# Kernel optimization log

Hardware: AMD Instinct MI355X
Metric: run time of the kernel (lower is better)

## Reference

```python
import jax, jax.numpy as jnp
import numpy as np

EPS = 1e-12


def _l2norm(v):
    return v / (jnp.linalg.norm(v) + EPS)


def _sn(W, u):
    """One-step power-iteration spectral normalization (torch spectral_norm, 1x1 conv weight).
    W: (out, in), u: (out,). u/v are treated as buffers (no grad)."""
    Wm = W.reshape(W.shape[0], -1)
    v = _l2norm(Wm.T @ u)
    u2 = _l2norm(Wm @ v)
    u2 = jax.lax.stop_gradient(u2)
    v = jax.lax.stop_gradient(v)
    sigma = u2 @ (Wm @ v)
    return W / sigma


def _maxpool2(x):
    # 2x2 max pool, stride 2, NCHW
    N, C, H, W = x.shape
    return x.reshape(N, C, H // 2, 2, W // 2, 2).max(axis=(3, 5))


def setup_inputs() -> dict:
    key = jax.random.key(0)
    ks = jax.random.split(key, 10)
    N, C, H, W = 16, 256, 64, 64
    s = 0.05  # keep logits moderate
    return {
        "x": jax.random.normal(ks[0], (N, C, H, W), dtype=jnp.float32),
        "Wt": jax.random.normal(ks[1], (C >> 3, C), dtype=jnp.float32) * s,
        "Wp": jax.random.normal(ks[2], (C >> 3, C), dtype=jnp.float32) * s,
        "Wg": jax.random.normal(ks[3], (C >> 1, C), dtype=jnp.float32) * s,
        "Wo": jax.random.normal(ks[4], (C, C >> 1), dtype=jnp.float32) * s,
        "ut": jax.random.normal(ks[5], (C >> 3,), dtype=jnp.float32),
        "up": jax.random.normal(ks[6], (C >> 3,), dtype=jnp.float32),
        "ug": jax.random.normal(ks[7], (C >> 1,), dtype=jnp.float32),
        "uo": jax.random.normal(ks[8], (C,), dtype=jnp.float32),
        "gamma": jnp.float32(0.1),  # nonzero so attention branch is exercised
    }


def reference(x, Wt, Wp, Wg, Wo, ut, up, ug, uo, gamma):
    N, C, H, W = x.shape
    L = H * W          # location_num
    Ld = L // 4        # downsampled_num
    # 1x1 convs as channel einsums with spectrally-normalized weights
    theta = jnp.einsum('oc,nchw->nohw', _sn(Wt, ut), x).reshape(N, C >> 3, L)
    phi = _maxpool2(jnp.einsum('oc,nchw->nohw', _sn(Wp, up), x)).reshape(N, C >> 3, Ld)
    attn = jax.nn.softmax(jnp.einsum('ncl,ncm->nlm', theta, phi), axis=-1)  # (N, L, Ld)
    g = _maxpool2(jnp.einsum('oc,nchw->nohw', _sn(Wg, ug), x)).reshape(N, C >> 1, Ld)
    attn_g = jnp.einsum('ncm,nlm->ncl', g, attn).reshape(N, C >> 1, H, W)
    attn_g = jnp.einsum('oc,nchw->nohw', _sn(Wo, uo), attn_g)
    return x + gamma * attn_g
```

## Files before the change

kernel.cpp:

```cpp
#include <hip/hip_runtime.h>
#include <math.h>

#define EPS 1e-12f

typedef unsigned short ushort_t;
typedef __attribute__((ext_vector_type(8))) short short8;
typedef __attribute__((ext_vector_type(4))) float f32x4;
typedef __attribute__((ext_vector_type(4))) unsigned short ushort4v;
typedef __attribute__((ext_vector_type(2))) unsigned int uint2v;

#define WS_WB_F 0
#define WS_WO_F 24576
#define WS_TH_F 40960
#define WS_PH_F 1089536
#define WS_G_F  1351680

__device__ __forceinline__ ushort_t f2bf(float f) {
  unsigned int u = __float_as_uint(f);
  u += 0x7fffu + ((u >> 16) & 1u);
  return (ushort_t)(u >> 16);
}
__device__ __forceinline__ float bf2f(ushort_t u) {
  return __uint_as_float(((unsigned int)u) << 16);
}
__device__ __forceinline__ unsigned int pack_bf2(float lo, float hi) {
  return (unsigned int)f2bf(lo) | ((unsigned int)f2bf(hi) << 16);
}

__device__ __forceinline__ void gload_lds16(const ushort_t* g, ushort_t* l) {
  __builtin_amdgcn_global_load_lds(
      (const __attribute__((address_space(1))) unsigned int*)g,
      (__attribute__((address_space(3))) unsigned int*)l, 16, 0, 0);
}

__device__ __forceinline__ float block_reduce_sum(float v, float* red) {
  int t = threadIdx.x;
  red[t] = v;
  __syncthreads();
  #pragma unroll
  for (int s = 128; s > 0; s >>= 1) {
    if (t < s) red[t] += red[t + s];
    __syncthreads();
  }
  float r = red[0];
  __syncthreads();
  return r;
}

__global__ __launch_bounds__(256) void sn_kernel(
    const float* __restrict__ Wt, const float* __restrict__ Wp,
    const float* __restrict__ Wg, const float* __restrict__ Wo,
    const float* __restrict__ ut, const float* __restrict__ up,
    const float* __restrict__ ug, const float* __restrict__ uo,
    float* __restrict__ ws) {
  __shared__ float red[256];
  __shared__ float ub[256];
  __shared__ float vb[256];
  const float* W; const float* u; int O, Ci;
  switch (blockIdx.x) {
    case 0:  W = Wt; u = ut; O = 32;  Ci = 256; break;
    case 1:  W = Wp; u = up; O = 32;  Ci = 256; break;
    case 2:  W = Wg; u = ug; O = 128; Ci = 256; break;
    default: W = Wo; u = uo; O = 256; Ci = 128; break;
  }
  int t = threadIdx.x;
  if (t < O) ub[t] = u[t];
  __syncthreads();
  float tv = 0.f;
  if (t < Ci) {
    for (int o = 0; o < O; o++) tv += W[o * Ci + t] * ub[o];
  }
  float nt2 = block_reduce_sum((t < Ci) ? tv * tv : 0.f, red);
  float ntn = sqrtf(nt2);
  if (t < Ci) vb[t] = tv / (ntn + EPS);
  __syncthreads();
  float sv = 0.f;
  if (t < O) {
    const float* Wr = W + (size_t)t * Ci;
    for (int c = 0; c < Ci; c += 4) {
      float4 wv = *(const float4*)(Wr + c);
      sv += wv.x * vb[c] + wv.y * vb[c + 1] + wv.z * vb[c + 2] + wv.w * vb[c + 3];
    }
  }
  float ss = block_reduce_sum((t < O) ? sv * sv : 0.f, red);
  float ns = sqrtf(ss);
  float sigma = ss / (ns + EPS);
  float inv = 1.f / sigma;
  int total = O * Ci;
  if (blockIdx.x == 3) {
    ushort_t* dst = (ushort_t*)(ws + WS_WO_F);
    for (int i = t; i < total; i += 256) {
      int o = i >> 7, c = i & 127;
      int oct = o >> 4, l16o = o & 15, kc = c >> 5, qd = (c >> 3) & 3, j = c & 7;
      dst[(((kc * 16 + oct) * 64 + qd * 16 + l16o) << 3) + j] = f2bf(W[i] * inv);
    }
  } else {
    int base_row = (blockIdx.x == 0) ? 0 : (blockIdx.x == 1 ? 32 : 64);
    ushort_t* dst = (ushort_t*)(ws + WS_WB_F);
    for (int i = t; i < total; i += 256) {
      int o = i >> 8, c = i & 255;
      int og = base_row + o;
      int mtg = og >> 4, l16o = og & 15, kc = c >> 5, qd = (c >> 3) & 3, j = c & 7;
      dst[(((mtg * 8 + kc) * 64 + qd * 16 + l16o) << 3) + j] = f2bf(W[i] * inv);
    }
  }
}

__global__ __launch_bounds__(256, 2) void proj_mfma(
    const float* __restrict__ x, const ushort_t* __restrict__ wb,
    ushort_t* __restrict__ theta_b, ushort_t* __restrict__ phi_b,
    ushort_t* __restrict__ g_b) {
  __shared__ ushort_t xb[128 * 264];
  const int t = threadIdx.x;
  const int n = blockIdx.y;
  const int l0 = blockIdx.x * 128;
  const float* xn = x + ((size_t)n * 256) * 4096 + l0;
  {
    const int lrel = t & 127;
    const int half = t >> 7;
    #pragma unroll 4
    for (int ch = 0; ch < 16; ++ch) {
      int chunk = half * 16 + ch;
      short8 v;
      #pragma unroll
      for (int j = 0; j < 8; ++j) {
        float f = xn[(size_t)(chunk * 8 + j) * 4096 + lrel];
        v[j] = (short)f2bf(f);
      }
      *(short8*)(&xb[lrel * 264 + chunk * 8]) = v;
    }
  }
  __syncthreads();
  const int w = t >> 6;
  const int lane = t & 63;
  const int quad = lane >> 4;
  const int l16 = lane & 15;
  const int rowA = (w * 16 + l16) * 264;
  const int rowB = (64 + w * 16 + l16) * 264;
  const int hd = blockIdx.x;
  #pragma unroll 1
  for (int pass = 0; pass < 2; ++pass) {
    f32x4 accA[6], accB[6];
    #pragma unroll
    for (int i = 0; i < 6; ++i) {
      accA[i] = (f32x4){0.f, 0.f, 0.f, 0.f};
      accB[i] = (f32x4){0.f, 0.f, 0.f, 0.f};
    }
    #pragma unroll
    for (int kc = 0; kc < 8; ++kc) {
      short8 bA = *(const short8*)(&xb[rowA + kc * 32 + quad * 8]);
      short8 bB = *(const short8*)(&xb[rowB + kc * 32 + quad * 8]);
      #pragma unroll
      for (int mt = 0; mt < 6; ++mt) {
        int mtg = pass * 6 + mt;
        short8 aW = *(const short8*)(wb + (((size_t)(mtg * 8 + kc) * 64 + lane) << 3));
        accA[mt] = __builtin_amdgcn_mfma_f32_16x16x32_bf16(aW, bA, accA[mt], 0, 0, 0);
        accB[mt] = __builtin_amdgcn_mfma_f32_16x16x32_bf16(aW, bB, accB[mt], 0, 0, 0);
      }
    }
    #pragma unroll
    for (int mt = 0; mt < 6; ++mt) {
      int mtg = pass * 6 + mt;
      if (mtg < 2) {
        int lA = l0 + w * 16 + l16;
        ushort4v vA, vB;
        #pragma unroll
        for (int r = 0; r < 4; ++r) { vA[r] = f2bf(accA[mt][r]); vB[r] = f2bf(accB[mt][r]); }
        *(ushort4v*)(theta_b + ((size_t)n * 4096 + lA) * 32 + mtg * 16 + quad * 4) = vA;
        *(ushort4v*)(theta_b + ((size_t)n * 4096 + lA + 64) * 32 + mtg * 16 + quad * 4) = vB;
      } else {
        float pm[4];
        #pragma unroll
        for (int r = 0; r < 4; ++r) {
          float v = fmaxf(accA[mt][r], accB[mt][r]);
          v = fmaxf(v, __shfl_xor(v, 1));
          pm[r] = v;
        }
        if ((l16 & 1) == 0) {
          int m = hd * 32 + w * 8 + (l16 >> 1);
          if (mtg < 4) {
            ushort4v vv;
            #pragma unroll
            for (int r = 0; r < 4; ++r) vv[r] = f2bf(pm[r]);
            *(ushort4v*)(phi_b + ((size_t)n * 1024 + m) * 32 + (mtg - 2) * 16 + quad * 4) = vv;
          } else {
            int cg0 = (mtg - 4) * 16 + quad * 4;
            #pragma unroll
            for (int r = 0; r < 4; ++r)
              g_b[((size_t)n * 128 + cg0 + r) * 1024 + m] = f2bf(pm[r]);
          }
        }
      }
    }
  }
}

__device__ __forceinline__ void stage_g(const ushort_t* gN, ushort_t* buf,
                                        int m0, int w, int l16, int quad) {
  #pragma unroll
  for (int b = 0; b < 8; ++b) {
    int idx = w * 8 + b;
    int j = idx >> 2, s = idx & 3;
    const ushort_t* src = gN + (size_t)(j * 16 + l16) * 1024 + m0 + s * 32 + quad * 8;
    gload_lds16(src, buf + (j * 4 + s) * 512);
  }
}

__device__ __forceinline__ void softmax_step(f32x4* st, float& M, float& L,
                                             f32x4* oa, unsigned int* pk) {
  f32x4 m4 = st[0];
  #pragma unroll
  for (int i = 1; i < 8; ++i) {
    #pragma unroll
    for (int r = 0; r < 4; ++r) m4[r] = fmaxf(m4[r], st[i][r]);
  }
  float mx = fmaxf(fmaxf(m4[0], m4[1]), fmaxf(m4[2], m4[3]));
  mx = fmaxf(mx, __shfl_xor(mx, 16));
  mx = fmaxf(mx, __shfl_xor(mx, 32));
  float nm = fmaxf(M, mx);
  float alpha = __expf(M - nm);
  M = nm;
  #pragma unroll
  for (int i = 0; i < 8; ++i) {
    #pragma unroll
    for (int r = 0; r < 4; ++r) st[i][r] = __expf(st[i][r] - nm);
  }
  f32x4 s4 = st[0];
  #pragma unroll
  for (int i = 1; i < 8; ++i) {
    #pragma unroll
    for (int r = 0; r < 4; ++r) s4[r] += st[i][r];
  }
  float ps = (s4[0] + s4[1]) + (s4[2] + s4[3]);
  ps += __shfl_xor(ps, 16);
  ps += __shfl_xor(ps, 32);
  L = L * alpha + ps;
  #pragma unroll
  for (int j = 0; j < 8; ++j) {
    #pragma unroll
    for (int r = 0; r < 4; ++r) oa[j][r] *= alpha;
  }
  #pragma unroll
  for (int i = 0; i < 8; ++i) {
    pk[2 * i]     = pack_bf2(st[i][0], st[i][1]);
    pk[2 * i + 1] = pack_bf2(st[i][2], st[i][3]);
  }
}

__global__ __launch_bounds__(256, 2) void attn_mfma(
    const float* __restrict__ x,
    const ushort_t* __restrict__ theta_b,
    const ushort_t* __restrict__ phi_b,
    const ushort_t* __restrict__ g_b,
    const ushort_t* __restrict__ Wo_fb,
    const float* __restrict__ gamma_p,
    float* __restrict__ out) {
  __shared__ __align__(16) unsigned char smem[77824];
  ushort_t* gbuf0 = (ushort_t*)smem;
  ushort_t* gbuf1 = (ushort_t*)(smem + 32768);
  ushort_t* outb  = (ushort_t*)smem;

  const int t = threadIdx.x;
  const int w = t >> 6;
  const int lane = t & 63;
  const int quad = lane >> 4;
  const int l16 = lane & 15;
  unsigned int* pw0 = (unsigned int*)(smem + 67584) + w * 640;
  unsigned int* pw1 = pw0 + 320;

  const int flat = blockIdx.y * 32 + blockIdx.x;
  const int nf = ((flat & 7) << 6) | (flat >> 3);
  const int n = nf >> 5;
  const int l0 = (nf & 31) << 7;
  const int lqw = l0 + w * 32;

  const short8 bth0 = *(const short8*)(theta_b + ((size_t)n * 4096 + lqw + l16) * 32 + quad * 8);
  const short8 bth1 = *(const short8*)(theta_b + ((size_t)n * 4096 + lqw + 16 + l16) * 32 + quad * 8);
  const ushort_t* phiN = phi_b + (size_t)n * 1024 * 32;
  const ushort_t* gN   = g_b + (size_t)n * 128 * 1024;

  f32x4 oacc0[8], oacc1[8];
  #pragma unroll
  for (int j = 0; j < 8; ++j) {
    oacc0[j] = (f32x4){0.f, 0.f, 0.f, 0.f};
    oacc1[j] = (f32x4){0.f, 0.f, 0.f, 0.f};
  }
  float M0 = -3.0e38f, L0v = 0.f, M1 = -3.0e38f, L1v = 0.f;

  stage_g(gN, gbuf0, 0, w, l16, quad);

  #pragma unroll 1
  for (int mc = 0; mc < 8; ++mc) {
    const int m0 = mc * 128;
    ushort_t* cbuf = (mc & 1) ? gbuf1 : gbuf0;
    ushort_t* nbuf = (mc & 1) ? gbuf0 : gbuf1;
    short8 aph[8];
    #pragma unroll
    for (int i = 0; i < 8; ++i)
      aph[i] = *(const short8*)(phiN + (size_t)(m0 + i * 16 + l16) * 32 + quad * 8);
    const f32x4 z = (f32x4){0.f, 0.f, 0.f, 0.f};
    f32x4 st0[8], st1[8];
    #pragma unroll
    for (int i = 0; i < 8; ++i) {
      st0[i] = __builtin_amdgcn_mfma_f32_16x16x32_bf16(aph[i], bth0, z, 0, 0, 0);
      st1[i] = __builtin_amdgcn_mfma_f32_16x16x32_bf16(aph[i], bth1, z, 0, 0, 0);
    }
    unsigned int pk0[16], pk1[16];
    softmax_step(st0, M0, L0v, oacc0, pk0);
    softmax_step(st1, M1, L1v, oacc1, pk1);
    __syncthreads();
    if (mc < 7) stage_g(gN, nbuf, m0 + 128, w, l16, quad);
    __builtin_amdgcn_s_setprio(1);
    #pragma unroll
    for (int s = 0; s < 4; ++s) {
      *(uint2v*)&pw0[l16 * 20 + quad * 2]     = (uint2v){pk0[4 * s],     pk0[4 * s + 1]};
      *(uint2v*)&pw0[l16 * 20 + 8 + quad * 2] = (uint2v){pk0[4 * s + 2], pk0[4 * s + 3]};
      *(uint2v*)&pw1[l16 * 20 + quad * 2]     = (uint2v){pk1[4 * s],     pk1[4 * s + 1]};
      *(uint2v*)&pw1[l16 * 20 + 8 + quad * 2] = (uint2v){pk1[4 * s + 2], pk1[4 * s + 3]};
      short8 pb0 = *(const short8*)&pw0[l16 * 20 + quad * 4];
      short8 pb1 = *(const short8*)&pw1[l16 * 20 + quad * 4];
      #pragma unroll
      for (int j = 0; j < 8; ++j) {
        short8 gf = *(const short8*)(cbuf + (size_t)(j * 4 + s) * 512 + lane * 8);
        oacc0[j] = __builtin_amdgcn_mfma_f32_16x16x32_bf16(gf, pb0, oacc0[j], 0, 0, 0);
        oacc1[j] = __builtin_amdgcn_mfma_f32_16x16x32_bf16(gf, pb1, oacc1[j], 0, 0, 0);
      }
    }
    __builtin_amdgcn_s_setprio(0);
  }
  __syncthreads();

  #pragma unroll
  for (int qg = 0; qg < 2; ++qg) {
    f32x4* oa = qg ? oacc1 : oacc0;
    unsigned int* pwq = qg ? pw1 : pw0;
    const float invL = 1.f / (qg ? L1v : L0v);
    f32x4 acc2[16];
    #pragma unroll
    for (int i = 0; i < 16; ++i) acc2[i] = (f32x4){0.f, 0.f, 0.f, 0.f};
    #pragma unroll
    for (int kc = 0; kc < 4; ++kc) {
      unsigned int e0 = pack_bf2(oa[2 * kc][0] * invL, oa[2 * kc][1] * invL);
      unsigned int e1 = pack_bf2(oa[2 * kc][2] * invL, oa[2 * kc][3] * invL);
      unsigned int e2 = pack_bf2(oa[2 * kc + 1][0] * invL, oa[2 * kc + 1][1] * invL);
      unsigned int e3 = pack_bf2(oa[2 * kc + 1][2] * invL, oa[2 * kc + 1][3] * invL);
      *(uint2v*)&pwq[l16 * 20 + quad * 2]     = (uint2v){e0, e1};
      *(uint2v*)&pwq[l16 * 20 + 8 + quad * 2] = (uint2v){e2, e3};
      short8 aO = *(const short8*)&pwq[l16 * 20 + quad * 4];
      #pragma unroll
      for (int oct = 0; oct < 16; ++oct) {
        short8 bw = *(const short8*)(Wo_fb + (((size_t)(kc * 16 + oct) * 64 + lane) << 3));
        acc2[oct] = __builtin_amdgcn_mfma_f32_16x16x32_bf16(aO, bw, acc2[oct], 0, 0, 0);
      }
    }
    #pragma unroll
    for (int oct = 0; oct < 16; ++oct) {
      #pragma unroll
      for (int r = 0; r < 4; ++r)
        outb[(oct * 16 + l16) * 132 + w * 32 + qg * 16 + quad * 4 + r] = f2bf(acc2[oct][r]);
    }
  }
  __syncthreads();
  {
    const float gm = gamma_p[0];
    const int lid = t & 31;
    const int ocr = t >> 5;
    #pragma unroll 8
    for (int ocg = 0; ocg < 32; ++ocg) {
      int row = ocg * 8 + ocr;
      ushort4v ov = *(const ushort4v*)(&outb[row * 132 + lid * 4]);
      const float* xp = x + ((size_t)n * 256 + row) * 4096 + l0 + lid * 4;
      float* op = out + ((size_t)n * 256 + row) * 4096 + l0 + lid * 4;
      float4 xv = *(const float4*)xp;
      float4 v;
      v.x = xv.x + gm * bf2f(ov[0]);
      v.y = xv.y + gm * bf2f(ov[1]);
      v.z = xv.z + gm * bf2f(ov[2]);
      v.w = xv.w + gm * bf2f(ov[3]);
      *(float4*)op = v;
    }
  }
}

extern "C" void kernel_launch(void* const* d_in, const int* in_sizes, int n_in,
                              void* d_out, int out_size, void* d_ws, size_t ws_size,
                              hipStream_t stream) {
  const float* x  = (const float*)d_in[0];
  const float* Wt = (const float*)d_in[1];
  const float* Wp = (const float*)d_in[2];
  const float* Wg = (const float*)d_in[3];
  const float* Wo = (const float*)d_in[4];
  const float* ut = (const float*)d_in[5];
  const float* up = (const float*)d_in[6];
  const float* ug = (const float*)d_in[7];
  const float* uo = (const float*)d_in[8];
  const float* gamma = (const float*)d_in[9];
  float* ws  = (float*)d_ws;
  float* out = (float*)d_out;

  ushort_t* wb      = (ushort_t*)(ws + WS_WB_F);
  ushort_t* Wo_b    = (ushort_t*)(ws + WS_WO_F);
  ushort_t* theta_b = (ushort_t*)(ws + WS_TH_F);
  ushort_t* phi_b   = (ushort_t*)(ws + WS_PH_F);
  ushort_t* g_b     = (ushort_t*)(ws + WS_G_F);

  sn_kernel<<<4, 256, 0, stream>>>(Wt, Wp, Wg, Wo, ut, up, ug, uo, ws);
  proj_mfma<<<dim3(32, 16), 256, 0, stream>>>(x, wb, theta_b, phi_b, g_b);
  attn_mfma<<<dim3(32, 16), 256, 0, stream>>>(x, theta_b, phi_b, g_b, Wo_b, gamma, out);
}
```

Before: 219.9 us.

## Permute phi and Wo layouts so MFMA outputs feed next MFMA directly in registers

Reorders how phi rows and the normalized Wo weight are stored so the accumulator layout of one MFMA matches the operand layout expected by the next. This removes the per-wave LDS round trip that transposed the packed softmax probabilities and the normalized attention output, and shrinks shared memory. It also loads phi operands inside the MFMA loop instead of preloading all eight. The risk is a permutation error in the K ordering that would silently corrupt results.

```diff
diff --git a/kernel.cpp b/kernel.cpp
--- a/kernel.cpp
+++ b/kernel.cpp
@@ -8,6 +8,7 @@
 typedef __attribute__((ext_vector_type(4))) float f32x4;
 typedef __attribute__((ext_vector_type(4))) unsigned short ushort4v;
 typedef __attribute__((ext_vector_type(2))) unsigned int uint2v;
+typedef __attribute__((ext_vector_type(4))) unsigned int uint32x4;
 
 #define WS_WB_F 0
 #define WS_WO_F 24576
@@ -91,8 +92,11 @@
     ushort_t* dst = (ushort_t*)(ws + WS_WO_F);
     for (int i = t; i < total; i += 256) {
       int o = i >> 7, c = i & 127;
-      int oct = o >> 4, l16o = o & 15, kc = c >> 5, qd = (c >> 3) & 3, j = c & 7;
-      dst[(((kc * 16 + oct) * 64 + qd * 16 + l16o) << 3) + j] = f2bf(W[i] * inv);
+      int oct = o >> 4, l16o = o & 15, kc = c >> 5, cl = c & 31;
+      int kap = (cl < 16) ? ((cl >> 2) * 8 + (cl & 3))
+                          : (((cl >> 2) & 3) * 8 + 4 + (cl & 3));
+      dst[(((kc * 16 + oct) * 64 + (kap >> 3) * 16 + l16o) << 3) + (kap & 7)] =
+          f2bf(W[i] * inv);
     }
   } else {
     int base_row = (blockIdx.x == 0) ? 0 : (blockIdx.x == 1 ? 32 : 64);
@@ -177,13 +181,15 @@
           pm[r] = v;
         }
         if ((l16 & 1) == 0) {
-          int m = hd * 32 + w * 8 + (l16 >> 1);
+          int rr = l16 >> 1;
           if (mtg < 4) {
+            int mp = hd * 32 + ((rr & 4) ? 16 : 0) + w * 4 + (rr & 3);
             ushort4v vv;
             #pragma unroll
             for (int r = 0; r < 4; ++r) vv[r] = f2bf(pm[r]);
-            *(ushort4v*)(phi_b + ((size_t)n * 1024 + m) * 32 + (mtg - 2) * 16 + quad * 4) = vv;
+            *(ushort4v*)(phi_b + ((size_t)n * 1024 + mp) * 32 + (mtg - 2) * 16 + quad * 4) = vv;
           } else {
+            int m = hd * 32 + w * 8 + rr;
             int cg0 = (mtg - 4) * 16 + quad * 4;
             #pragma unroll
             for (int r = 0; r < 4; ++r)
@@ -201,8 +207,8 @@
   for (int b = 0; b < 8; ++b) {
     int idx = w * 8 + b;
     int j = idx >> 2, s = idx & 3;
-    const ushort_t* src = gN + (size_t)(j * 16 + l16) * 1024 + m0 + s * 32 + quad * 8;
-    gload_lds16(src, buf + (j * 4 + s) * 512);
+    gload_lds16(gN + (size_t)(j * 16 + l16) * 1024 + m0 + s * 32 + quad * 8,
+                buf + (j * 4 + s) * 512);
   }
 }
 
@@ -255,7 +261,7 @@
     const ushort_t* __restrict__ Wo_fb,
     const float* __restrict__ gamma_p,
     float* __restrict__ out) {
-  __shared__ __align__(16) unsigned char smem[77824];
+  __shared__ __align__(16) unsigned char smem[67584];
   ushort_t* gbuf0 = (ushort_t*)smem;
   ushort_t* gbuf1 = (ushort_t*)(smem + 32768);
   ushort_t* outb  = (ushort_t*)smem;
@@ -265,8 +271,6 @@
   const int lane = t & 63;
   const int quad = lane >> 4;
   const int l16 = lane & 15;
-  unsigned int* pw0 = (unsigned int*)(smem + 67584) + w * 640;
-  unsigned int* pw1 = pw0 + 320;
 
   const int flat = blockIdx.y * 32 + blockIdx.x;
   const int nf = ((flat & 7) << 6) | (flat >> 3);
@@ -294,16 +298,13 @@
     const int m0 = mc * 128;
     ushort_t* cbuf = (mc & 1) ? gbuf1 : gbuf0;
     ushort_t* nbuf = (mc & 1) ? gbuf0 : gbuf1;
-    short8 aph[8];
-    #pragma unroll
-    for (int i = 0; i < 8; ++i)
-      aph[i] = *(const short8*)(phiN + (size_t)(m0 + i * 16 + l16) * 32 + quad * 8);
     const f32x4 z = (f32x4){0.f, 0.f, 0.f, 0.f};
     f32x4 st0[8], st1[8];
     #pragma unroll
     for (int i = 0; i < 8; ++i) {
-      st0[i] = __builtin_amdgcn_mfma_f32_16x16x32_bf16(aph[i], bth0, z, 0, 0, 0);
-      st1[i] = __builtin_amdgcn_mfma_f32_16x16x32_bf16(aph[i], bth1, z, 0, 0, 0);
+      short8 aph = *(const short8*)(phiN + (size_t)(m0 + i * 16 + l16) * 32 + quad * 8);
+      st0[i] = __builtin_amdgcn_mfma_f32_16x16x32_bf16(aph, bth0, z, 0, 0, 0);
+      st1[i] = __builtin_amdgcn_mfma_f32_16x16x32_bf16(aph, bth1, z, 0, 0, 0);
     }
     unsigned int pk0[16], pk1[16];
     softmax_step(st0, M0, L0v, oacc0, pk0);
@@ -313,12 +314,10 @@
     __builtin_amdgcn_s_setprio(1);
     #pragma unroll
     for (int s = 0; s < 4; ++s) {
-      *(uint2v*)&pw0[l16 * 20 + quad * 2]     = (uint2v){pk0[4 * s],     pk0[4 * s + 1]};
-      *(uint2v*)&pw0[l16 * 20 + 8 + quad * 2] = (uint2v){pk0[4 * s + 2], pk0[4 * s + 3]};
-      *(uint2v*)&pw1[l16 * 20 + quad * 2]     = (uint2v){pk1[4 * s],     pk1[4 * s + 1]};
-      *(uint2v*)&pw1[l16 * 20 + 8 + quad * 2] = (uint2v){pk1[4 * s + 2], pk1[4 * s + 3]};
-      short8 pb0 = *(const short8*)&pw0[l16 * 20 + quad * 4];
-      short8 pb1 = *(const short8*)&pw1[l16 * 20 + quad * 4];
+      uint32x4 u0 = {pk0[4 * s], pk0[4 * s + 1], pk0[4 * s + 2], pk0[4 * s + 3]};
+      uint32x4 u1 = {pk1[4 * s], pk1[4 * s + 1], pk1[4 * s + 2], pk1[4 * s + 3]};
+      short8 pb0 = __builtin_bit_cast(short8, u0);
+      short8 pb1 = __builtin_bit_cast(short8, u1);
       #pragma unroll
       for (int j = 0; j < 8; ++j) {
         short8 gf = *(const short8*)(cbuf + (size_t)(j * 4 + s) * 512 + lane * 8);
@@ -333,20 +332,18 @@
   #pragma unroll
   for (int qg = 0; qg < 2; ++qg) {
     f32x4* oa = qg ? oacc1 : oacc0;
-    unsigned int* pwq = qg ? pw1 : pw0;
     const float invL = 1.f / (qg ? L1v : L0v);
     f32x4 acc2[16];
     #pragma unroll
     for (int i = 0; i < 16; ++i) acc2[i] = (f32x4){0.f, 0.f, 0.f, 0.f};
     #pragma unroll
     for (int kc = 0; kc < 4; ++kc) {
-      unsigned int e0 = pack_bf2(oa[2 * kc][0] * invL, oa[2 * kc][1] * invL);
-      unsigned int e1 = pack_bf2(oa[2 * kc][2] * invL, oa[2 * kc][3] * invL);
-      unsigned int e2 = pack_bf2(oa[2 * kc + 1][0] * invL, oa[2 * kc + 1][1] * invL);
-      unsigned int e3 = pack_bf2(oa[2 * kc + 1][2] * invL, oa[2 * kc + 1][3] * invL);
-      *(uint2v*)&pwq[l16 * 20 + quad * 2]     = (uint2v){e0, e1};
-      *(uint2v*)&pwq[l16 * 20 + 8 + quad * 2] = (uint2v){e2, e3};
-      short8 aO = *(const short8*)&pwq[l16 * 20 + quad * 4];
+      uint32x4 u;
+      u[0] = pack_bf2(oa[2 * kc][0] * invL, oa[2 * kc][1] * invL);
+      u[1] = pack_bf2(oa[2 * kc][2] * invL, oa[2 * kc][3] * invL);
+      u[2] = pack_bf2(oa[2 * kc + 1][0] * invL, oa[2 * kc + 1][1] * invL);
+      u[3] = pack_bf2(oa[2 * kc + 1][2] * invL, oa[2 * kc + 1][3] * invL);
+      short8 aO = __builtin_bit_cast(short8, u);
       #pragma unroll
       for (int oct = 0; oct < 16; ++oct) {
         short8 bw = *(const short8*)(Wo_fb + (((size_t)(kc * 16 + oct) * 64 + lane) << 3));
```

Result: no change. 217.4 us (-1.1%).
